# Performance work log

Hardware: AMD Instinct MI355X
Metric: run time of the kernel (lower is better)

## Reference

```python
import jax, jax.numpy as jnp
import numpy as np

NUM_HEADS = 8
NUM_GROUPS = 32
EPS = 1e-5


def setup_inputs() -> dict:
    key = jax.random.key(0)
    ks = jax.random.split(key, 7)
    B, C, H, W = 16, 512, 32, 32
    x = jax.random.normal(ks[0], (B, C, H, W), dtype=jnp.float32)
    gn_gamma = jnp.ones((C,), dtype=jnp.float32)
    gn_beta = jnp.zeros((C,), dtype=jnp.float32)
    # Conv1d with kernel_size=1 is a per-position matmul: weight [out, in]
    qkv_w = jax.random.normal(ks[1], (3 * C, C), dtype=jnp.float32) / np.sqrt(C)
    qkv_b = jax.random.normal(ks[2], (3 * C,), dtype=jnp.float32) * 0.01
    proj_w = jax.random.normal(ks[3], (C, C), dtype=jnp.float32) / np.sqrt(C)
    proj_b = jax.random.normal(ks[4], (C,), dtype=jnp.float32) * 0.01
    return {"x": x, "gn_gamma": gn_gamma, "gn_beta": gn_beta,
            "qkv_w": qkv_w, "qkv_b": qkv_b, "proj_w": proj_w, "proj_b": proj_b}


def group_norm(x, gamma, beta):
    # x: [B, C, H, W]
    B, C, H, W = x.shape
    xg = x.reshape(B, NUM_GROUPS, C // NUM_GROUPS, H, W)
    mean = xg.mean(axis=(2, 3, 4), keepdims=True)
    var = xg.var(axis=(2, 3, 4), keepdims=True)
    xg = (xg - mean) * jax.lax.rsqrt(var + EPS)
    x = xg.reshape(B, C, H, W)
    return x * gamma[None, :, None, None] + beta[None, :, None, None]


def reference(x, gn_gamma, gn_beta, qkv_w, qkv_b, proj_w, proj_b):
    B, C, H, W = x.shape
    N = H * W
    hd = C // NUM_HEADS  # head dim
    h = group_norm(x, gn_gamma, gn_beta).reshape(B, C, N)
    # 1x1 Conv1d == matmul over channel dim
    qkv = jnp.einsum('oc,bcn->bon', qkv_w, h) + qkv_b[None, :, None]
    qkv = qkv.reshape(B, 3, NUM_HEADS, hd, N)
    q, k, v = qkv[:, 0], qkv[:, 1], qkv[:, 2]  # each [B, h, d, N]
    scale = hd ** (-0.5)
    attn = jnp.einsum('bhdn,bhdm->bhnm', q, k) * scale  # [B, h, N, N]
    attn = jax.nn.softmax(attn, axis=-1)
    out = jnp.einsum('bhnm,bhdm->bhdn', attn, v).reshape(B, C, N)
    out = jnp.einsum('oc,bcn->bon', proj_w, out) + proj_b[None, :, None]
    return x + out.reshape(B, C, H, W)
```

## Files before the change

### kernel.cpp

```cpp
#include <hip/hip_runtime.h>

typedef unsigned short u16;
typedef unsigned int u32;
typedef __bf16 bf16x8 __attribute__((ext_vector_type(8)));
typedef float f32x4 __attribute__((ext_vector_type(4)));
typedef float f32x16 __attribute__((ext_vector_type(16)));

#define B_ 16
#define C_ 512
#define N_ 1024
#define NB_ 16384
#define K_ 512
#define M3_ 1536
#define SCALE_Q 0.18033688011112042f

__device__ __forceinline__ u16 f2bf(float f) {
  u32 u = __float_as_uint(f);
  u32 r = (u + 0x7FFFu + ((u >> 16) & 1u)) >> 16;
  return (u16)r;
}

__device__ __forceinline__ void gl_lds16(const void* g, void* l) {
  __builtin_amdgcn_global_load_lds(
      (const __attribute__((address_space(1))) u32*)(uintptr_t)g,
      (__attribute__((address_space(3))) u32*)(u32)(uintptr_t)l, 16, 0, 0);
}

__device__ __forceinline__ u32 cvtpk(float lo, float hi) {
  u32 r;
  asm("v_cvt_pk_bf16_f32 %0, %1, %2" : "=v"(r) : "v"(lo), "v"(hi));
  return r;
}

__device__ __forceinline__ float exp2a(float x) {
  float r;
  asm("v_exp_f32 %0, %1" : "=v"(r) : "v"(x));
  return r;
}

__device__ __forceinline__ void plswap2(u32& a, u32& b) {
#if __has_builtin(__builtin_amdgcn_permlane32_swap)
  auto r = __builtin_amdgcn_permlane32_swap((int)a, (int)b, false, false);
  a = (u32)r[0];
  b = (u32)r[1];
#else
  asm("v_permlane32_swap_b32 %0, %1" : "+v"(a), "+v"(b));
#endif
}

__device__ __forceinline__ float xhalf_sum(float x) {
  u32 a = __float_as_uint(x), b = a;
  plswap2(a, b);
  return __uint_as_float(a) + __uint_as_float(b);
}

__device__ __forceinline__ int swz(int row) {
  return (row & 7) ^ (((row >> 3) & 1) << 2);
}

__global__ __launch_bounds__(256) void cast_bf16_kernel(const float* __restrict__ src,
                                                        u16* __restrict__ dst, int n) {
  int i = blockIdx.x * 256 + threadIdx.x;
  if (i < n) dst[i] = f2bf(src[i]);
}

__global__ __launch_bounds__(256) void gnorm_kernel(const float* __restrict__ x,
                                                    const float* __restrict__ gamma,
                                                    const float* __restrict__ beta,
                                                    u16* __restrict__ ht) {
  int blk = blockIdx.x;
  int b = blk >> 5, g = blk & 31;
  int t = threadIdx.x;
  const float* xb = x + ((size_t)(b * C_ + g * 16) << 10);
  float v[16][4];
  float s = 0.f, sq = 0.f;
#pragma unroll
  for (int cc = 0; cc < 16; ++cc) {
#pragma unroll
    for (int r = 0; r < 4; ++r) {
      float f = xb[cc * 1024 + r * 256 + t];
      v[cc][r] = f; s += f; sq += f * f;
    }
  }
#pragma unroll
  for (int m = 32; m >= 1; m >>= 1) { s += __shfl_xor(s, m, 64); sq += __shfl_xor(sq, m, 64); }
  __shared__ float red[8];
  int w = t >> 6;
  if ((t & 63) == 0) { red[w * 2] = s; red[w * 2 + 1] = sq; }
  __syncthreads();
  s = red[0] + red[2] + red[4] + red[6];
  sq = red[1] + red[3] + red[5] + red[7];
  float mean = s * (1.f / 16384.f);
  float var = sq * (1.f / 16384.f) - mean * mean;
  float rstd = rsqrtf(var + 1e-5f);
  float gm[16], bt[16];
#pragma unroll
  for (int cc = 0; cc < 16; ++cc) {
    gm[cc] = gamma[g * 16 + cc] * rstd;
    bt[cc] = beta[g * 16 + cc];
  }
  u16* hb = ht + ((size_t)(b << 10)) * C_ + g * 16;
#pragma unroll
  for (int r = 0; r < 4; ++r) {
    u32 pk[8];
#pragma unroll
    for (int q = 0; q < 8; ++q) {
      float f0 = (v[2 * q][r] - mean) * gm[2 * q] + bt[2 * q];
      float f1 = (v[2 * q + 1][r] - mean) * gm[2 * q + 1] + bt[2 * q + 1];
      pk[q] = (u32)f2bf(f0) | ((u32)f2bf(f1) << 16);
    }
    u16* dp = hb + (size_t)(r * 256 + t) * C_;
    uint4 a = {pk[0], pk[1], pk[2], pk[3]};
    uint4 b4 = {pk[4], pk[5], pk[6], pk[7]};
    *(uint4*)dp = a;
    *(uint4*)(dp + 8) = b4;
  }
}

template <int EPI>
__global__ __launch_bounds__(256) void gemm_kernel(const u16* __restrict__ A,
                                                   const u16* __restrict__ BT,
                                                   const float* __restrict__ bias,
                                                   u16* __restrict__ Co,
                                                   const float* __restrict__ xres,
                                                   float* __restrict__ Fo) {
  __shared__ u16 ldsA[128 * 64];
  __shared__ u16 ldsB[128 * 64];
  int t = threadIdx.x;
  int l = t & 63, w = t >> 6;
  int wr = w >> 1, wc = w & 1;
  int ro0 = blockIdx.y * 128, co0 = blockIdx.x * 128;
  f32x4 acc[4][4];
#pragma unroll
  for (int m = 0; m < 4; ++m)
#pragma unroll
    for (int n = 0; n < 4; ++n) acc[m][n] = {0.f, 0.f, 0.f, 0.f};
  int srow = t >> 3, sg = t & 7;
  for (int kt = 0; kt < 8; ++kt) {
    int k0 = kt * 64;
#pragma unroll
    for (int i = 0; i < 4; ++i) {
      int row = i * 32 + srow;
      int gl = sg ^ (row & 7);
      gl_lds16(A + (size_t)(ro0 + row) * K_ + k0 + gl * 8, ldsA + (i * 32 + w * 8) * 64);
      gl_lds16(BT + (size_t)(co0 + row) * K_ + k0 + gl * 8, ldsB + (i * 32 + w * 8) * 64);
    }
    __syncthreads();
#pragma unroll
    for (int ks = 0; ks < 2; ++ks) {
      bf16x8 af[4], bfr[4];
#pragma unroll
      for (int m = 0; m < 4; ++m) {
        int row = wr * 64 + m * 16 + (l & 15);
        int ph = (ks * 4 + (l >> 4)) ^ (row & 7);
        af[m] = *(const bf16x8*)&ldsA[row * 64 + ph * 8];
      }
#pragma unroll
      for (int n = 0; n < 4; ++n) {
        int row = wc * 64 + n * 16 + (l & 15);
        int ph = (ks * 4 + (l >> 4)) ^ (row & 7);
        bfr[n] = *(const bf16x8*)&ldsB[row * 64 + ph * 8];
      }
#pragma unroll
      for (int m = 0; m < 4; ++m)
#pragma unroll
        for (int n = 0; n < 4; ++n)
          acc[m][n] = __builtin_amdgcn_mfma_f32_16x16x32_bf16(af[m], bfr[n], acc[m][n], 0, 0, 0);
    }
    __syncthreads();
  }
#pragma unroll
  for (int m = 0; m < 4; ++m) {
#pragma unroll
    for (int j = 0; j < 4; ++j) {
      int row = ro0 + wr * 64 + m * 16 + (l >> 4) * 4 + j;
      float bv = bias[row];
#pragma unroll
      for (int n = 0; n < 4; ++n) {
        int col = co0 + wc * 64 + n * 16 + (l & 15);
        float val = acc[m][n][j] + bv;
        if (EPI == 0) {
          if (row < C_) val *= SCALE_Q;
          Co[(size_t)row * NB_ + col] = f2bf(val);
        } else {
          int bb = col >> 10, nn = col & 1023;
          size_t oi = (((size_t)(bb * C_ + row)) << 10) + nn;
          Fo[oi] = xres[oi] + val;
        }
      }
    }
  }
}

__global__ __launch_bounds__(256) void transpose_qk_kernel(const u16* __restrict__ qkv,
                                                           u16* __restrict__ qT,
                                                           u16* __restrict__ kT) {
  int blk = blockIdx.x;
  int nt = blk & 15, h = (blk >> 4) & 7, sel = (blk >> 7) & 1, b = blk >> 8;
  const u16* src = qkv + (size_t)(sel * C_ + h * 64) * NB_ + (b << 10) + nt * 64;
  u16* dst = (sel ? kT : qT) + ((size_t)((b * 8 + h) << 10) + nt * 64) * 64;
  __shared__ u16 tile[64][68];
  int t = threadIdx.x;
  int r = t >> 2, c0 = (t & 3) * 16;
  const u16* sp = src + (size_t)r * NB_ + c0;
  uint4 a = *(const uint4*)sp;
  uint4 bb = *(const uint4*)(sp + 8);
  u16* tp = &tile[r][c0];
  uint2 t0 = {a.x, a.y}, t1 = {a.z, a.w}, t2 = {bb.x, bb.y}, t3 = {bb.z, bb.w};
  *(uint2*)tp = t0; *(uint2*)(tp + 4) = t1; *(uint2*)(tp + 8) = t2; *(uint2*)(tp + 12) = t3;
  __syncthreads();
  u32 pk[8];
#pragma unroll
  for (int q = 0; q < 8; ++q)
    pk[q] = (u32)tile[c0 + 2 * q][r] | ((u32)tile[c0 + 2 * q + 1][r] << 16);
  u16* dp = dst + (size_t)r * 64 + c0;
  uint4 o0 = {pk[0], pk[1], pk[2], pk[3]};
  uint4 o1 = {pk[4], pk[5], pk[6], pk[7]};
  *(uint4*)dp = o0;
  *(uint4*)(dp + 8) = o1;
}

__global__ __launch_bounds__(128) void attn_kernel(const u16* __restrict__ qT,
                                                   const u16* __restrict__ kT,
                                                   const u16* __restrict__ qkv,
                                                   u16* __restrict__ aoT) {
  __shared__ u16 lds[2][2][64 * 64];
  int bid = blockIdx.x;
  int wid = (bid & 7) * 128 + (bid >> 3);
  int qt = wid & 7, h = (wid >> 3) & 7, b = wid >> 6;
  int bh = b * 8 + h;
  int t = threadIdx.x, l = t & 63, w = t >> 6;
  int lq = l & 31, hi = l >> 5;
  int q0 = qt * 128 + w * 64;

  bf16x8 qf[2][4];
#pragma unroll
  for (int qg = 0; qg < 2; ++qg) {
    const u16* qbase = qT + ((size_t)(bh << 10) + q0 + qg * 32 + lq) * 64 + hi * 8;
#pragma unroll
    for (int kc = 0; kc < 4; ++kc) qf[qg][kc] = *(const bf16x8*)(qbase + kc * 16);
  }

  f32x16 accO[2][2];
#pragma unroll
  for (int qg = 0; qg < 2; ++qg)
#pragma unroll
    for (int dt = 0; dt < 2; ++dt)
#pragma unroll
      for (int r = 0; r < 16; ++r) accO[qg][dt][r] = 0.f;
  float lsum[2] = {0.f, 0.f};

  const u16* kbase = kT + ((size_t)(bh << 10)) * 64;
  const u16* vbase = qkv + (size_t)(2 * C_ + h * 64) * NB_ + (b << 10);

  auto stage = [&](int buf, int mt) {
    int kv0 = mt * 64;
#pragma unroll
    for (int r = 0; r < 4; ++r) {
      int flat = r * 128 + w * 64 + l;
      int row = flat >> 3, g = flat & 7;
      int gs = (g ^ swz(row)) * 8;
      gl_lds16(kbase + (size_t)(kv0 + row) * 64 + gs, &lds[buf][0][(r * 128 + w * 64) * 8]);
      gl_lds16(vbase + (size_t)row * NB_ + kv0 + gs, &lds[buf][1][(r * 128 + w * 64) * 8]);
    }
  };

  auto step = [&](int cur, int mt) {
    if (mt < 15) stage(cur ^ 1, mt + 1);
    const u16* Kl = lds[cur][0];
    const u16* Vl = lds[cur][1];
    f32x16 sc[2][2];
#pragma unroll
    for (int c = 0; c < 2; ++c) {
      int kk = c * 32 + lq;
      int sw = swz(kk);
#pragma unroll
      for (int r = 0; r < 16; ++r) { sc[0][c][r] = 0.f; sc[1][c][r] = 0.f; }
#pragma unroll
      for (int kc = 0; kc < 4; ++kc) {
        int p = (2 * kc + hi) ^ sw;
        bf16x8 kf = *(const bf16x8*)(Kl + kk * 64 + p * 8);
        sc[0][c] = __builtin_amdgcn_mfma_f32_32x32x16_bf16(kf, qf[0][kc], sc[0][c], 0, 0, 0);
        sc[1][c] = __builtin_amdgcn_mfma_f32_32x32x16_bf16(kf, qf[1][kc], sc[1][c], 0, 0, 0);
      }
    }
    u32 pfu[2][4][4];
#pragma unroll
    for (int qg = 0; qg < 2; ++qg) {
      float ps = 0.f;
#pragma unroll
      for (int c = 0; c < 2; ++c)
#pragma unroll
        for (int r = 0; r < 16; ++r) {
          float e = exp2a(sc[qg][c][r]);
          sc[qg][c][r] = e;
          ps += e;
        }
      lsum[qg] += ps;
#pragma unroll
      for (int c = 0; c < 2; ++c) {
        u32 pk[8];
#pragma unroll
        for (int p = 0; p < 8; ++p) pk[p] = cvtpk(sc[qg][c][2 * p], sc[qg][c][2 * p + 1]);
#pragma unroll
        for (int cc = 0; cc < 2; ++cc) {
          u32 w0 = pk[cc * 4 + 0], w2 = pk[cc * 4 + 2];
          u32 w1 = pk[cc * 4 + 1], w3 = pk[cc * 4 + 3];
          plswap2(w0, w2);
          plswap2(w1, w3);
          int kcc = c * 2 + cc;
          pfu[qg][kcc][0] = w0; pfu[qg][kcc][1] = w1;
          pfu[qg][kcc][2] = w2; pfu[qg][kcc][3] = w3;
        }
      }
    }
#pragma unroll
    for (int kcc = 0; kcc < 4; ++kcc) {
#pragma unroll
      for (int dt = 0; dt < 2; ++dt) {
        int d = dt * 32 + lq;
        int p = (2 * kcc + hi) ^ swz(d);
        bf16x8 vf = *(const bf16x8*)(Vl + d * 64 + p * 8);
        union { u32 u[4]; bf16x8 v; } pf0, pf1;
        pf0.u[0] = pfu[0][kcc][0]; pf0.u[1] = pfu[0][kcc][1];
        pf0.u[2] = pfu[0][kcc][2]; pf0.u[3] = pfu[0][kcc][3];
        pf1.u[0] = pfu[1][kcc][0]; pf1.u[1] = pfu[1][kcc][1];
        pf1.u[2] = pfu[1][kcc][2]; pf1.u[3] = pfu[1][kcc][3];
        accO[0][dt] = __builtin_amdgcn_mfma_f32_32x32x16_bf16(vf, pf0.v, accO[0][dt], 0, 0, 0);
        accO[1][dt] = __builtin_amdgcn_mfma_f32_32x32x16_bf16(vf, pf1.v, accO[1][dt], 0, 0, 0);
      }
    }
    __syncthreads();
  };

  stage(0, 0);
  __syncthreads();
#pragma unroll 1
  for (int mt2 = 0; mt2 < 8; ++mt2) {
    step(0, mt2 * 2);
    step(1, mt2 * 2 + 1);
  }

#pragma unroll
  for (int qg = 0; qg < 2; ++qg) {
    float inv = 1.0f / xhalf_sum(lsum[qg]);
    u16* ob = aoT + ((size_t)((b << 10) + q0 + qg * 32 + lq)) * C_ + h * 64;
#pragma unroll
    for (int dt = 0; dt < 2; ++dt)
#pragma unroll
      for (int rg = 0; rg < 4; ++rg) {
        int d0 = dt * 32 + rg * 8 + hi * 4;
        u32 w0 = cvtpk(accO[qg][dt][rg * 4 + 0] * inv, accO[qg][dt][rg * 4 + 1] * inv);
        u32 w1 = cvtpk(accO[qg][dt][rg * 4 + 2] * inv, accO[qg][dt][rg * 4 + 3] * inv);
        uint2 o = {w0, w1};
        *(uint2*)(ob + d0) = o;
      }
  }
}

extern "C" void kernel_launch(void* const* d_in, const int* in_sizes, int n_in,
                              void* d_out, int out_size, void* d_ws, size_t ws_size,
                              hipStream_t stream) {
  const float* x = (const float*)d_in[0];
  const float* gamma = (const float*)d_in[1];
  const float* beta = (const float*)d_in[2];
  const float* qkv_w = (const float*)d_in[3];
  const float* qkv_b = (const float*)d_in[4];
  const float* proj_w = (const float*)d_in[5];
  const float* proj_b = (const float*)d_in[6];
  float* out = (float*)d_out;
  char* ws = (char*)d_ws;
  u16* wq = (u16*)(ws);
  u16* wp = (u16*)(ws + 1572864);
  u16* ht = (u16*)(ws + 2097152);
  u16* qkvo = (u16*)(ws + 18874368);
  u16* qT = (u16*)(ws + 69206016);
  u16* kT = (u16*)(ws + 85983232);
  u16* aoT = ht;

  cast_bf16_kernel<<<3072, 256, 0, stream>>>(qkv_w, wq, M3_ * K_);
  cast_bf16_kernel<<<1024, 256, 0, stream>>>(proj_w, wp, C_ * K_);
  gnorm_kernel<<<512, 256, 0, stream>>>(x, gamma, beta, ht);
  gemm_kernel<0><<<dim3(128, 12), 256, 0, stream>>>(wq, ht, qkv_b, qkvo, nullptr, nullptr);
  transpose_qk_kernel<<<4096, 256, 0, stream>>>(qkvo, qT, kT);
  attn_kernel<<<1024, 128, 0, stream>>>(qT, kT, qkvo, aoT);
  gemm_kernel<1><<<dim3(128, 4), 256, 0, stream>>>(wp, aoT, proj_b, nullptr, x, out);
}
```

Baseline: 138.7 us.

## Fuse Q/K transpose into QKV GEMM epilogue and per-wave pipeline attention

The QKV GEMM epilogue now writes Q (pre-scaled) and K directly in the transposed [b,h,n,d] layout, which removes the separate transpose kernel and its extra round trip through global memory. The attention kernel is restructured so each wave stages its own K/V tiles of 32 keys into private LDS double buffers. It waits on s_waitcnt vmcnt instead of block-wide __syncthreads, uses new XOR swizzles, and raises wave priority with s_setprio around MFMA bursts. In exchange, the GEMM epilogue does scattered 8-byte stores, and each wave now loads K/V separately, which duplicates global traffic across the two waves.

```diff
diff --git a/kernel.cpp b/kernel.cpp
--- a/kernel.cpp
+++ b/kernel.cpp
@@ -52,10 +52,6 @@
   u32 a = __float_as_uint(x), b = a;
   plswap2(a, b);
   return __uint_as_float(a) + __uint_as_float(b);
-}
-
-__device__ __forceinline__ int swz(int row) {
-  return (row & 7) ^ (((row >> 3) & 1) << 2);
 }
 
 __global__ __launch_bounds__(256) void cast_bf16_kernel(const float* __restrict__ src,
@@ -122,6 +118,8 @@
                                                    const u16* __restrict__ BT,
                                                    const float* __restrict__ bias,
                                                    u16* __restrict__ Co,
+                                                   u16* __restrict__ qTo,
+                                                   u16* __restrict__ kTo,
                                                    const float* __restrict__ xres,
                                                    float* __restrict__ Fo) {
   __shared__ u16 ldsA[128 * 64];
@@ -169,69 +167,69 @@
     }
     __syncthreads();
   }
-#pragma unroll
-  for (int m = 0; m < 4; ++m) {
-#pragma unroll
-    for (int j = 0; j < 4; ++j) {
-      int row = ro0 + wr * 64 + m * 16 + (l >> 4) * 4 + j;
-      float bv = bias[row];
+  if (EPI == 0 && ro0 < 1024) {
+    int sel = ro0 >> 9;
+    u16* dstb = sel ? kTo : qTo;
+    float scl = sel ? 1.f : SCALE_Q;
+#pragma unroll
+    for (int m = 0; m < 4; ++m) {
+      int row0 = ro0 + wr * 64 + m * 16 + (l >> 4) * 4;
+      int o = row0 & 511;
+      int h = o >> 6, d0 = o & 63;
+      float bv0 = bias[row0], bv1 = bias[row0 + 1];
+      float bv2 = bias[row0 + 2], bv3 = bias[row0 + 3];
 #pragma unroll
       for (int n = 0; n < 4; ++n) {
         int col = co0 + wc * 64 + n * 16 + (l & 15);
-        float val = acc[m][n][j] + bv;
-        if (EPI == 0) {
-          if (row < C_) val *= SCALE_Q;
-          Co[(size_t)row * NB_ + col] = f2bf(val);
-        } else {
-          int bb = col >> 10, nn = col & 1023;
-          size_t oi = (((size_t)(bb * C_ + row)) << 10) + nn;
-          Fo[oi] = xres[oi] + val;
+        int bb = col >> 10, nn = col & 1023;
+        float v0 = (acc[m][n][0] + bv0) * scl;
+        float v1 = (acc[m][n][1] + bv1) * scl;
+        float v2 = (acc[m][n][2] + bv2) * scl;
+        float v3 = (acc[m][n][3] + bv3) * scl;
+        uint2 ov = {cvtpk(v0, v1), cvtpk(v2, v3)};
+        *(uint2*)(dstb + ((size_t)((bb * 8 + h) << 10) + nn) * 64 + d0) = ov;
+      }
+    }
+  } else {
+#pragma unroll
+    for (int m = 0; m < 4; ++m) {
+#pragma unroll
+      for (int j = 0; j < 4; ++j) {
+        int row = ro0 + wr * 64 + m * 16 + (l >> 4) * 4 + j;
+        float bv = bias[row];
+#pragma unroll
+        for (int n = 0; n < 4; ++n) {
+          int col = co0 + wc * 64 + n * 16 + (l & 15);
+          float val = acc[m][n][j] + bv;
+          if (EPI == 0) {
+            Co[(size_t)row * NB_ + col] = f2bf(val);
+          } else {
+            int bb = col >> 10, nn = col & 1023;
+            size_t oi = (((size_t)(bb * C_ + row)) << 10) + nn;
+            Fo[oi] = xres[oi] + val;
+          }
         }
       }
     }
   }
-}
-
-__global__ __launch_bounds__(256) void transpose_qk_kernel(const u16* __restrict__ qkv,
-                                                           u16* __restrict__ qT,
-                                                           u16* __restrict__ kT) {
-  int blk = blockIdx.x;
-  int nt = blk & 15, h = (blk >> 4) & 7, sel = (blk >> 7) & 1, b = blk >> 8;
-  const u16* src = qkv + (size_t)(sel * C_ + h * 64) * NB_ + (b << 10) + nt * 64;
-  u16* dst = (sel ? kT : qT) + ((size_t)((b * 8 + h) << 10) + nt * 64) * 64;
-  __shared__ u16 tile[64][68];
-  int t = threadIdx.x;
-  int r = t >> 2, c0 = (t & 3) * 16;
-  const u16* sp = src + (size_t)r * NB_ + c0;
-  uint4 a = *(const uint4*)sp;
-  uint4 bb = *(const uint4*)(sp + 8);
-  u16* tp = &tile[r][c0];
-  uint2 t0 = {a.x, a.y}, t1 = {a.z, a.w}, t2 = {bb.x, bb.y}, t3 = {bb.z, bb.w};
-  *(uint2*)tp = t0; *(uint2*)(tp + 4) = t1; *(uint2*)(tp + 8) = t2; *(uint2*)(tp + 12) = t3;
-  __syncthreads();
-  u32 pk[8];
-#pragma unroll
-  for (int q = 0; q < 8; ++q)
-    pk[q] = (u32)tile[c0 + 2 * q][r] | ((u32)tile[c0 + 2 * q + 1][r] << 16);
-  u16* dp = dst + (size_t)r * 64 + c0;
-  uint4 o0 = {pk[0], pk[1], pk[2], pk[3]};
-  uint4 o1 = {pk[4], pk[5], pk[6], pk[7]};
-  *(uint4*)dp = o0;
-  *(uint4*)(dp + 8) = o1;
 }
 
 __global__ __launch_bounds__(128) void attn_kernel(const u16* __restrict__ qT,
                                                    const u16* __restrict__ kT,
                                                    const u16* __restrict__ qkv,
                                                    u16* __restrict__ aoT) {
-  __shared__ u16 lds[2][2][64 * 64];
+  __shared__ u16 Kall[2][2][2048];
+  __shared__ u16 Vall[2][2][2048];
   int bid = blockIdx.x;
   int wid = (bid & 7) * 128 + (bid >> 3);
-  int qt = wid & 7, h = (wid >> 3) & 7, b = wid >> 6;
+  int qt2 = wid & 7, h = (wid >> 3) & 7, b = wid >> 6;
   int bh = b * 8 + h;
   int t = threadIdx.x, l = t & 63, w = t >> 6;
   int lq = l & 31, hi = l >> 5;
-  int q0 = qt * 128 + w * 64;
+  int q0 = qt2 * 128 + w * 64;
+
+  u16* Kw = &Kall[w][0][0];
+  u16* Vw = &Vall[w][0][0];
 
   bf16x8 qf[2][4];
 #pragma unroll
@@ -250,96 +248,106 @@
       for (int r = 0; r < 16; ++r) accO[qg][dt][r] = 0.f;
   float lsum[2] = {0.f, 0.f};
 
-  const u16* kbase = kT + ((size_t)(bh << 10)) * 64;
-  const u16* vbase = qkv + (size_t)(2 * C_ + h * 64) * NB_ + (b << 10);
-
-  auto stage = [&](int buf, int mt) {
-    int kv0 = mt * 64;
-#pragma unroll
-    for (int r = 0; r < 4; ++r) {
-      int flat = r * 128 + w * 64 + l;
-      int row = flat >> 3, g = flat & 7;
-      int gs = (g ^ swz(row)) * 8;
-      gl_lds16(kbase + (size_t)(kv0 + row) * 64 + gs, &lds[buf][0][(r * 128 + w * 64) * 8]);
-      gl_lds16(vbase + (size_t)row * NB_ + kv0 + gs, &lds[buf][1][(r * 128 + w * 64) * 8]);
-    }
+  const u16* k_src = kT + ((size_t)(bh << 10) + (l >> 3)) * 64 + (((l & 7) ^ ((l >> 3) & 7)) * 8);
+  const u16* v_src = qkv + (size_t)(2 * C_ + h * 64 + (l >> 2)) * NB_ + (b << 10) +
+                     (((l & 3) ^ ((l >> 3) & 3)) * 8);
+
+  const u16* kfp[4];
+#pragma unroll
+  for (int kc = 0; kc < 4; ++kc)
+    kfp[kc] = Kw + lq * 64 + (((2 * kc + hi) ^ (lq & 7)) * 8);
+  const u16* vfp[4];
+#pragma unroll
+  for (int dt = 0; dt < 2; ++dt)
+#pragma unroll
+    for (int kcc = 0; kcc < 2; ++kcc)
+      vfp[dt * 2 + kcc] = Vw + (dt * 32 + lq) * 32 + (((kcc * 2 + hi) ^ ((lq >> 1) & 3)) * 8);
+
+  auto stage = [&](int buf) {
+    u16* Kd = Kw + buf * 2048;
+    u16* Vd = Vw + buf * 2048;
+#pragma unroll
+    for (int i = 0; i < 4; ++i) gl_lds16(k_src + i * 512, Kd + i * 512);
+#pragma unroll
+    for (int i = 0; i < 4; ++i) gl_lds16(v_src + (size_t)i * 16 * NB_, Vd + i * 512);
+    k_src += 2048;
+    v_src += 32;
   };
 
-  auto step = [&](int cur, int mt) {
-    if (mt < 15) stage(cur ^ 1, mt + 1);
-    const u16* Kl = lds[cur][0];
-    const u16* Vl = lds[cur][1];
-    f32x16 sc[2][2];
-#pragma unroll
-    for (int c = 0; c < 2; ++c) {
-      int kk = c * 32 + lq;
-      int sw = swz(kk);
-#pragma unroll
-      for (int r = 0; r < 16; ++r) { sc[0][c][r] = 0.f; sc[1][c][r] = 0.f; }
-#pragma unroll
-      for (int kc = 0; kc < 4; ++kc) {
-        int p = (2 * kc + hi) ^ sw;
-        bf16x8 kf = *(const bf16x8*)(Kl + kk * 64 + p * 8);
-        sc[0][c] = __builtin_amdgcn_mfma_f32_32x32x16_bf16(kf, qf[0][kc], sc[0][c], 0, 0, 0);
-        sc[1][c] = __builtin_amdgcn_mfma_f32_32x32x16_bf16(kf, qf[1][kc], sc[1][c], 0, 0, 0);
-      }
-    }
-    u32 pfu[2][4][4];
+  auto step = [&](int buf, bool dostage) {
+    if (dostage) {
+      stage(buf ^ 1);
+      asm volatile("s_waitcnt vmcnt(8)" ::: "memory");
+    } else {
+      asm volatile("s_waitcnt vmcnt(0)" ::: "memory");
+    }
+    __builtin_amdgcn_sched_barrier(0);
+    bf16x8 kf[4], vf[4];
+#pragma unroll
+    for (int kc = 0; kc < 4; ++kc) kf[kc] = *(const bf16x8*)(kfp[kc] + buf * 2048);
+#pragma unroll
+    for (int j = 0; j < 4; ++j) vf[j] = *(const bf16x8*)(vfp[j] + buf * 2048);
+    f32x16 sc[2];
+#pragma unroll
+    for (int qg = 0; qg < 2; ++qg)
+#pragma unroll
+      for (int r = 0; r < 16; ++r) sc[qg][r] = 0.f;
+    __builtin_amdgcn_s_setprio(1);
+#pragma unroll
+    for (int kc = 0; kc < 4; ++kc) {
+      sc[0] = __builtin_amdgcn_mfma_f32_32x32x16_bf16(kf[kc], qf[0][kc], sc[0], 0, 0, 0);
+      sc[1] = __builtin_amdgcn_mfma_f32_32x32x16_bf16(kf[kc], qf[1][kc], sc[1], 0, 0, 0);
+    }
+    __builtin_amdgcn_s_setprio(0);
+    u32 pfu[2][2][4];
 #pragma unroll
     for (int qg = 0; qg < 2; ++qg) {
       float ps = 0.f;
 #pragma unroll
-      for (int c = 0; c < 2; ++c)
-#pragma unroll
-        for (int r = 0; r < 16; ++r) {
-          float e = exp2a(sc[qg][c][r]);
-          sc[qg][c][r] = e;
-          ps += e;
+      for (int r = 0; r < 16; ++r) {
+        float e = exp2a(sc[qg][r]);
+        sc[qg][r] = e;
+        ps += e;
+      }
+      lsum[qg] += ps;
+      u32 pk[8];
+#pragma unroll
+      for (int p = 0; p < 8; ++p) pk[p] = cvtpk(sc[qg][2 * p], sc[qg][2 * p + 1]);
+#pragma unroll
+      for (int cc = 0; cc < 2; ++cc) {
+        u32 w0 = pk[cc * 4 + 0], w2 = pk[cc * 4 + 2];
+        u32 w1 = pk[cc * 4 + 1], w3 = pk[cc * 4 + 3];
+        plswap2(w0, w2);
+        plswap2(w1, w3);
+        pfu[qg][cc][0] = w0; pfu[qg][cc][1] = w1;
+        pfu[qg][cc][2] = w2; pfu[qg][cc][3] = w3;
+      }
+    }
+    __builtin_amdgcn_s_setprio(1);
+#pragma unroll
+    for (int kcc = 0; kcc < 2; ++kcc)
+#pragma unroll
+      for (int dt = 0; dt < 2; ++dt) {
+        bf16x8 vv = vf[dt * 2 + kcc];
+#pragma unroll
+        for (int qg = 0; qg < 2; ++qg) {
+          union { u32 u[4]; bf16x8 v; } pf;
+          pf.u[0] = pfu[qg][kcc][0]; pf.u[1] = pfu[qg][kcc][1];
+          pf.u[2] = pfu[qg][kcc][2]; pf.u[3] = pfu[qg][kcc][3];
+          accO[qg][dt] = __builtin_amdgcn_mfma_f32_32x32x16_bf16(vv, pf.v, accO[qg][dt], 0, 0, 0);
         }
-      lsum[qg] += ps;
-#pragma unroll
-      for (int c = 0; c < 2; ++c) {
-        u32 pk[8];
-#pragma unroll
-        for (int p = 0; p < 8; ++p) pk[p] = cvtpk(sc[qg][c][2 * p], sc[qg][c][2 * p + 1]);
-#pragma unroll
-        for (int cc = 0; cc < 2; ++cc) {
-          u32 w0 = pk[cc * 4 + 0], w2 = pk[cc * 4 + 2];
-          u32 w1 = pk[cc * 4 + 1], w3 = pk[cc * 4 + 3];
-          plswap2(w0, w2);
-          plswap2(w1, w3);
-          int kcc = c * 2 + cc;
-          pfu[qg][kcc][0] = w0; pfu[qg][kcc][1] = w1;
-          pfu[qg][kcc][2] = w2; pfu[qg][kcc][3] = w3;
-        }
-      }
-    }
-#pragma unroll
-    for (int kcc = 0; kcc < 4; ++kcc) {
-#pragma unroll
-      for (int dt = 0; dt < 2; ++dt) {
-        int d = dt * 32 + lq;
-        int p = (2 * kcc + hi) ^ swz(d);
-        bf16x8 vf = *(const bf16x8*)(Vl + d * 64 + p * 8);
-        union { u32 u[4]; bf16x8 v; } pf0, pf1;
-        pf0.u[0] = pfu[0][kcc][0]; pf0.u[1] = pfu[0][kcc][1];
-        pf0.u[2] = pfu[0][kcc][2]; pf0.u[3] = pfu[0][kcc][3];
-        pf1.u[0] = pfu[1][kcc][0]; pf1.u[1] = pfu[1][kcc][1];
-        pf1.u[2] = pfu[1][kcc][2]; pf1.u[3] = pfu[1][kcc][3];
-        accO[0][dt] = __builtin_amdgcn_mfma_f32_32x32x16_bf16(vf, pf0.v, accO[0][dt], 0, 0, 0);
-        accO[1][dt] = __builtin_amdgcn_mfma_f32_32x32x16_bf16(vf, pf1.v, accO[1][dt], 0, 0, 0);
-      }
-    }
-    __syncthreads();
+      }
+    __builtin_amdgcn_s_setprio(0);
   };
 
-  stage(0, 0);
-  __syncthreads();
+  stage(0);
 #pragma unroll 1
-  for (int mt2 = 0; mt2 < 8; ++mt2) {
-    step(0, mt2 * 2);
-    step(1, mt2 * 2 + 1);
-  }
+  for (int s = 0; s < 15; ++s) {
+    step(0, true);
+    step(1, true);
+  }
+  step(0, true);
+  step(1, false);
 
 #pragma unroll
   for (int qg = 0; qg < 2; ++qg) {
@@ -381,8 +389,7 @@
   cast_bf16_kernel<<<3072, 256, 0, stream>>>(qkv_w, wq, M3_ * K_);
   cast_bf16_kernel<<<1024, 256, 0, stream>>>(proj_w, wp, C_ * K_);
   gnorm_kernel<<<512, 256, 0, stream>>>(x, gamma, beta, ht);
-  gemm_kernel<0><<<dim3(128, 12), 256, 0, stream>>>(wq, ht, qkv_b, qkvo, nullptr, nullptr);
-  transpose_qk_kernel<<<4096, 256, 0, stream>>>(qkvo, qT, kT);
+  gemm_kernel<0><<<dim3(128, 12), 256, 0, stream>>>(wq, ht, qkv_b, qkvo, qT, kT, nullptr, nullptr);
   attn_kernel<<<1024, 128, 0, stream>>>(qT, kT, qkvo, aoT);
-  gemm_kernel<1><<<dim3(128, 4), 256, 0, stream>>>(wp, aoT, proj_b, nullptr, x, out);
-}
+  gemm_kernel<1><<<dim3(128, 4), 256, 0, stream>>>(wp, aoT, proj_b, nullptr, nullptr, nullptr, x, out);
+}
```

After: 135.4 us. -2.4%, faster.
